# Kernel tuning notes

Hardware: AMD Instinct MI355X
Metric: run time of the kernel (lower is better)

Reference implementation:

```python
import jax, jax.numpy as jnp
import numpy as np

D = 1024
H = 16
HD = D // H
FF = 4 * D
LN_EPS = 1e-5


def _layernorm(x, w, b):
    mu = jnp.mean(x, axis=-1, keepdims=True)
    var = jnp.mean(jnp.square(x - mu), axis=-1, keepdims=True)
    return (x - mu) * jax.lax.rsqrt(var + LN_EPS) * w + b


def setup_inputs() -> dict:
    key = jax.random.key(0)
    ks = jax.random.split(key, 12)
    s = 0.02
    return {
        "x": jax.random.normal(ks[0], (8, 1024, D), jnp.float32),
        "c": jax.random.normal(ks[1], (8, D), jnp.float32),
        "ln1_w": jnp.ones((D,), jnp.float32),
        "ln1_b": jnp.zeros((D,), jnp.float32),
        "ln2_w": jnp.ones((D,), jnp.float32),
        "ln2_b": jnp.zeros((D,), jnp.float32),
        "ada_w": jax.random.normal(ks[2], (D, 6 * D), jnp.float32) * s,
        "ada_b": jnp.zeros((6 * D,), jnp.float32),
        "qkv_w": jax.random.normal(ks[3], (D, 3 * D), jnp.float32) * s,
        "qkv_b": jnp.zeros((3 * D,), jnp.float32),
        "proj_w": jax.random.normal(ks[4], (D, D), jnp.float32) * s,
        "proj_b": jnp.zeros((D,), jnp.float32),
        "fc1_w": jax.random.normal(ks[5], (D, FF), jnp.float32) * s,
        "fc1_b": jnp.zeros((FF,), jnp.float32),
        "fc2_w": jax.random.normal(ks[6], (FF, D), jnp.float32) * s,
        "fc2_b": jnp.zeros((D,), jnp.float32),
    }


def reference(x, c, ln1_w, ln1_b, ln2_w, ln2_b, ada_w, ada_b,
              qkv_w, qkv_b, proj_w, proj_b, fc1_w, fc1_b, fc2_w, fc2_b):
    B, L, _ = x.shape
    # adaLN modulation: SiLU(c) @ W -> 6 chunks of (B, D)
    ssg = jax.nn.silu(c) @ ada_w + ada_b
    msa_shift, msa_scale, msa_gate, mlp_shift, mlp_scale, mlp_gate = jnp.split(ssg, 6, axis=-1)

    def modulate(h, shift, scale):
        return h * (1.0 + scale[:, None, :]) + shift[:, None, :]

    # ---- attention branch ----
    h = modulate(_layernorm(x, ln1_w, ln1_b), msa_shift, msa_scale)
    qkv = h @ qkv_w + qkv_b                      # (B, L, 3D)
    q, k, v = jnp.split(qkv, 3, axis=-1)
    q = q.reshape(B, L, H, HD).transpose(0, 2, 1, 3)   # (B, H, L, HD)
    k = k.reshape(B, L, H, HD).transpose(0, 2, 1, 3)
    v = v.reshape(B, L, H, HD).transpose(0, 2, 1, 3)
    scores = jnp.einsum("bhqd,bhkd->bhqk", q, k) / jnp.sqrt(jnp.float32(HD))
    attn = jax.nn.softmax(scores, axis=-1)
    a = jnp.einsum("bhqk,bhkd->bhqd", attn, v)   # (B, H, L, HD)
    a = a.transpose(0, 2, 1, 3).reshape(B, L, D)
    a = a @ proj_w + proj_b
    x = x + msa_gate[:, None, :] * a

    # ---- MLP branch ----
    h = modulate(_layernorm(x, ln2_w, ln2_b), mlp_shift, mlp_scale)
    h = jax.nn.gelu(h @ fc1_w + fc1_b, approximate=True)
    h = h @ fc2_w + fc2_b
    x = x + mlp_gate[:, None, :] * h
    return x
```

## Files before the change

### kernel.cpp

```cpp
#include <hip/hip_runtime.h>
#include <math.h>

#define DMODEL 1024
#define SIXD   6144
#define NHEAD  16
#define HEADD  64
#define LSEQ   1024
#define NBATCH 8
#define MROWS  8192

typedef unsigned short ushort_t;
typedef __attribute__((ext_vector_type(8))) short bf16x8;
typedef __attribute__((ext_vector_type(4))) float f32x4;

__device__ __forceinline__ unsigned short f2bf(float f) {
  unsigned int u = __float_as_uint(f);
  u += 0x7fff + ((u >> 16) & 1);
  return (unsigned short)(u >> 16);
}

__device__ __forceinline__ void gload_lds16(const void* g, void* l) {
  __builtin_amdgcn_global_load_lds(
      (const __attribute__((address_space(1))) unsigned int*)g,
      (__attribute__((address_space(3))) unsigned int*)l, 16, 0, 0);
}

__global__ void tcast_kernel(const float* __restrict__ W, ushort_t* __restrict__ WT,
                             int K, int N) {
  __shared__ float tile[32][33];
  int tx = threadIdx.x & 31, ty = threadIdx.x >> 5;
  int n0 = blockIdx.x * 32, k0 = blockIdx.y * 32;
#pragma unroll
  for (int r = 0; r < 4; ++r)
    tile[ty + 8*r][tx] = W[(size_t)(k0 + ty + 8*r) * N + n0 + tx];
  __syncthreads();
#pragma unroll
  for (int r = 0; r < 4; ++r)
    WT[(size_t)(n0 + ty + 8*r) * K + k0 + tx] = f2bf(tile[tx][ty + 8*r]);
}

__global__ __launch_bounds__(256) void vtrans_kernel(
    const ushort_t* __restrict__ qkvb, ushort_t* __restrict__ vT) {
  __shared__ ushort_t tile[128][66];
  int bh = blockIdx.x;
  int kt = blockIdx.y;
  int b = bh >> 4, h = bh & 15;
  int tid = threadIdx.x;
#pragma unroll
  for (int i = 0; i < 4; ++i) {
    int flat = tid + 256 * i;
    int r = flat >> 3, c8 = flat & 7;
    bf16x8 v = *(const bf16x8*)((const short*)qkvb +
        (size_t)(b * LSEQ + kt * 128 + r) * 3072 + 2048 + h * 64 + c8 * 8);
#pragma unroll
    for (int j = 0; j < 8; ++j) tile[r][c8 * 8 + j] = (ushort_t)v[j];
  }
  __syncthreads();
#pragma unroll
  for (int i = 0; i < 4; ++i) {
    int d = i * 16 + (tid >> 4);
    int kc = tid & 15;
    bf16x8 ov;
#pragma unroll
    for (int j = 0; j < 8; ++j) ov[j] = (short)tile[kc * 8 + j][d];
    *(bf16x8*)((short*)vT + (size_t)(bh * 64 + d) * 1024 + kt * 128 + kc * 8) = ov;
  }
}

__global__ void ada_kernel(const float* __restrict__ c, const float* __restrict__ ada_w,
                           const float* __restrict__ ada_b, float* __restrict__ ssg) {
  __shared__ float s[DMODEL];
  int b = blockIdx.y;
  int j = blockIdx.x * 256 + threadIdx.x;
  for (int i = threadIdx.x; i < DMODEL; i += 256) {
    float v = c[b * DMODEL + i];
    s[i] = v / (1.0f + __expf(-v));
  }
  __syncthreads();
  float acc = ada_b[j];
#pragma unroll 8
  for (int k = 0; k < DMODEL; ++k)
    acc = fmaf(s[k], ada_w[(size_t)k * SIXD + j], acc);
  ssg[b * SIXD + j] = acc;
}

__global__ __launch_bounds__(256) void ln_mod_kernel(
    const float* __restrict__ xin, const float* __restrict__ lw,
    const float* __restrict__ lb, const float* __restrict__ ssg,
    int shift_off, int scale_off, ushort_t* __restrict__ outB) {
  int row = blockIdx.x;
  int b = row >> 10;
  int tid = threadIdx.x;
  float4 v = ((const float4*)xin)[(size_t)row * 256 + tid];
  float sum = v.x + v.y + v.z + v.w;
  float sq  = v.x*v.x + v.y*v.y + v.z*v.z + v.w*v.w;
#pragma unroll
  for (int m = 32; m; m >>= 1) { sum += __shfl_xor(sum, m); sq += __shfl_xor(sq, m); }
  __shared__ float rbuf[8];
  int w = tid >> 6, lane = tid & 63;
  if (lane == 0) { rbuf[w] = sum; rbuf[4 + w] = sq; }
  __syncthreads();
  sum = rbuf[0] + rbuf[1] + rbuf[2] + rbuf[3];
  sq  = rbuf[4] + rbuf[5] + rbuf[6] + rbuf[7];
  float mu  = sum * (1.0f / 1024.0f);
  float var = sq * (1.0f / 1024.0f) - mu * mu;
  float rs  = rsqrtf(var + 1e-5f);
  const float* sg = ssg + b * SIXD;
  float vv[4] = {v.x, v.y, v.z, v.w};
  ushort4 pk;
  unsigned short* pks = (unsigned short*)&pk;
#pragma unroll
  for (int j = 0; j < 4; ++j) {
    int d = tid * 4 + j;
    float h = (vv[j] - mu) * rs * lw[d] + lb[d];
    h = h * (1.0f + sg[scale_off + d]) + sg[shift_off + d];
    pks[j] = f2bf(h);
  }
  ((ushort4*)outB)[(size_t)row * 256 + tid] = pk;
}

template <int EPI>
__global__ __launch_bounds__(256, 2) void gemm_kernel(
    const ushort_t* __restrict__ A, const ushort_t* __restrict__ BT,
    const float* __restrict__ bias, const float* __restrict__ ssg,
    const float* resid, float* outF, ushort_t* __restrict__ outB,
    int N, int K, int gate_off, int gxs) {
  __shared__ __align__(16) char SM[65536];
  int tid = threadIdx.x, lane = tid & 63, w = tid >> 6;
  int l15 = lane & 15, g = lane >> 4;
  int orig = blockIdx.x;
  int xcd = orig & 7;
  int idx = orig >> 3;
  int bxi = idx & ((1 << gxs) - 1);
  int byl = (idx >> gxs) & 7;
  int bxg = idx >> (gxs + 3);
  int bx = (bxg << gxs) + bxi;
  int by = (xcd << 3) + byl;
  int m0 = by * 128, n0 = bx * 128;
  int wrow = (w >> 1) * 64, wcol = (w & 1) * 64;
  f32x4 zero = {0.f, 0.f, 0.f, 0.f};
  f32x4 acc[4][4];
#pragma unroll
  for (int i = 0; i < 4; ++i)
#pragma unroll
    for (int j = 0; j < 4; ++j) acc[i][j] = zero;

  const char* asrc[4];
  const char* bsrc[4];
#pragma unroll
  for (int ch = 0; ch < 4; ++ch) {
    int flat = ch * 4096 + tid * 16;
    int row = flat >> 7;
    int colb = (flat & 127) ^ ((row & 7) << 4);
    asrc[ch] = (const char*)A  + ((size_t)(m0 + row) * K) * 2 + colb;
    bsrc[ch] = (const char*)BT + ((size_t)(n0 + row) * K) * 2 + colb;
  }

  int T = K >> 6;
#pragma unroll
  for (int ch = 0; ch < 4; ++ch)
    gload_lds16(asrc[ch], SM + ch * 4096 + tid * 16);
#pragma unroll
  for (int ch = 0; ch < 4; ++ch)
    gload_lds16(bsrc[ch], SM + 16384 + ch * 4096 + tid * 16);

  for (int t = 0; t < T; ++t) {
    if (t + 1 < T) {
      char* base = SM + ((t + 1) & 1) * 32768;
      size_t ko = (size_t)(t + 1) * 128;
#pragma unroll
      for (int ch = 0; ch < 4; ++ch)
        gload_lds16(asrc[ch] + ko, base + ch * 4096 + tid * 16);
#pragma unroll
      for (int ch = 0; ch < 4; ++ch)
        gload_lds16(bsrc[ch] + ko, base + 16384 + ch * 4096 + tid * 16);
      asm volatile("s_waitcnt vmcnt(8)" ::: "memory");
    } else {
      asm volatile("s_waitcnt vmcnt(0)" ::: "memory");
    }
    asm volatile("s_barrier" ::: "memory");
    const char* ab = SM + (t & 1) * 32768;
    const char* bb = ab + 16384;
#pragma unroll
    for (int kk = 0; kk < 2; ++kk) {
      bf16x8 af[4], bfr[4];
#pragma unroll
      for (int i = 0; i < 4; ++i) {
        int ar = wrow + i * 16 + l15;
        af[i]  = *(const bf16x8*)(ab + ar * 128 + ((kk * 64 + g * 16) ^ ((ar & 7) << 4)));
        int br = wcol + i * 16 + l15;
        bfr[i] = *(const bf16x8*)(bb + br * 128 + ((kk * 64 + g * 16) ^ ((br & 7) << 4)));
      }
#pragma unroll
      for (int i = 0; i < 4; ++i)
#pragma unroll
        for (int j = 0; j < 4; ++j)
          acc[i][j] = __builtin_amdgcn_mfma_f32_16x16x32_bf16(af[i], bfr[j], acc[i][j], 0, 0, 0);
    }
    asm volatile("s_barrier" ::: "memory");
  }
#pragma unroll
  for (int i = 0; i < 4; ++i)
#pragma unroll
    for (int j = 0; j < 4; ++j)
#pragma unroll
      for (int r = 0; r < 4; ++r) {
        int grow = m0 + wrow + i * 16 + g * 4 + r;
        int gcol = n0 + wcol + j * 16 + l15;
        float v = acc[i][j][r] + bias[gcol];
        if (EPI == 0) {
          outB[(size_t)grow * N + gcol] = f2bf(v);
        } else if (EPI == 1 || EPI == 3) {
          int bb2 = grow >> 10;
          float gate = ssg[bb2 * SIXD + gate_off + gcol];
          size_t idx2 = (size_t)grow * N + gcol;
          outF[idx2] = resid[idx2] + gate * v;
        } else {
          float u = v;
          float t2 = 0.7978845608028654f * (u + 0.044715f * u * u * u);
          float e = __expf(2.0f * t2);
          float th = 1.0f - 2.0f / (e + 1.0f);
          outB[(size_t)grow * N + gcol] = f2bf(0.5f * u * (1.0f + th));
        }
      }
}

__global__ __launch_bounds__(256, 2) void attn_kernel(
    const ushort_t* __restrict__ qkv,
    const ushort_t* __restrict__ vT,
    ushort_t* __restrict__ aout) {
  __shared__ __align__(16) char SM[33024];
  float* lbuf = (float*)(SM + 32768);
  int tid = threadIdx.x, lane = tid & 63, w = tid >> 6;
  int l15 = lane & 15, g = lane >> 4;
  int qt = blockIdx.x, bh = blockIdx.y;
  int b = bh >> 4, h = bh & 15;
  const float sc = 0.18033688f;

  bf16x8 aq[2], aq2[2];
  {
    int qrow = qt * 128 + w * 16 + l15;
    const short* qp = (const short*)qkv + (size_t)(b * LSEQ + qrow) * 3072 + h * 64 + g * 8;
    aq[0] = *(const bf16x8*)qp;
    aq[1] = *(const bf16x8*)(qp + 32);
    const short* qp2 = qp + (size_t)64 * 3072;
    aq2[0] = *(const bf16x8*)qp2;
    aq2[1] = *(const bf16x8*)(qp2 + 32);
#pragma unroll
    for (int ks = 0; ks < 2; ++ks) {
#pragma unroll
      for (int s = 0; s < 2; ++s) {
        union { bf16x8 v; unsigned short u[8]; } qi, qo;
        qi.v = s ? aq2[ks] : aq[ks];
#pragma unroll
        for (int j = 0; j < 8; j += 2) {
          float lo = __uint_as_float((unsigned)qi.u[j] << 16) * sc;
          float hi = __uint_as_float((unsigned)qi.u[j + 1] << 16) * sc;
          unsigned pkd;
          asm("v_cvt_pk_bf16_f32 %0, %1, %2" : "=v"(pkd) : "v"(lo), "v"(hi));
          qo.u[j] = (unsigned short)(pkd & 0xffff);
          qo.u[j + 1] = (unsigned short)(pkd >> 16);
        }
        if (s) aq2[ks] = qo.v; else aq[ks] = qo.v;
      }
    }
  }

  const char* ksrc[2];
  const char* vsrc[2];
#pragma unroll
  for (int p = 0; p < 2; ++p) {
    int flat = p * 4096 + w * 1024 + lane * 16;
    int row = flat >> 7;
    int colb = (flat & 127) ^ ((row & 7) << 4);
    ksrc[p] = (const char*)qkv + ((size_t)(b * LSEQ + row) * 3072 + 1024 + h * 64) * 2 + colb;
    vsrc[p] = (const char*)vT + ((size_t)(bh * 64 + row) * 1024) * 2 + colb;
  }

  f32x4 zero = {0.f, 0.f, 0.f, 0.f};
  f32x4 o[4] = {zero, zero, zero, zero};
  f32x4 o2[4] = {zero, zero, zero, zero};
  float lrow = 0.f, lrow2 = 0.f;

#pragma unroll
  for (int p = 0; p < 2; ++p) {
    gload_lds16(ksrc[p], SM + p * 4096 + w * 1024);
    gload_lds16(vsrc[p], SM + 16384 + p * 4096 + w * 1024);
  }
  __syncthreads();

  for (int t = 0; t < 16; ++t) {
    int cur = t & 1;
    if (t < 15) {
      size_t koff = (size_t)(t + 1) * (64 * 3072 * 2);
      size_t voff = (size_t)(t + 1) * 128;
#pragma unroll
      for (int p = 0; p < 2; ++p) {
        gload_lds16(ksrc[p] + koff, SM + (cur ^ 1) * 8192 + p * 4096 + w * 1024);
        gload_lds16(vsrc[p] + voff, SM + 16384 + (cur ^ 1) * 8192 + p * 4096 + w * 1024);
      }
    }
    f32x4 s4[4] = {zero, zero, zero, zero};
    f32x4 s4b[4] = {zero, zero, zero, zero};
    __builtin_amdgcn_s_setprio(1);
#pragma unroll
    for (int c = 0; c < 4; ++c)
#pragma unroll
      for (int ks = 0; ks < 2; ++ks) {
        int key = c * 16 + l15;
        bf16x8 ak = *(const bf16x8*)(SM + cur * 8192 + key * 128 +
                                     ((ks * 64 + g * 16) ^ ((key & 7) << 4)));
        s4[c]  = __builtin_amdgcn_mfma_f32_16x16x32_bf16(ak, aq[ks],  s4[c],  0, 0, 0);
        s4b[c] = __builtin_amdgcn_mfma_f32_16x16x32_bf16(ak, aq2[ks], s4b[c], 0, 0, 0);
      }
    __builtin_amdgcn_s_setprio(0);
    unsigned pa[2][4], pa2[2][4];
    int gl = (g & 1) * 2;
#pragma unroll
    for (int s = 0; s < 2; ++s) {
      float p16[16], sump = 0.f;
#pragma unroll
      for (int c = 0; c < 4; ++c)
#pragma unroll
        for (int r = 0; r < 4; ++r) {
          float p = exp2f(s ? s4b[c][r] : s4[c][r]);
          p16[c * 4 + r] = p;
          sump += p;
        }
      sump += __shfl_xor(sump, 16);
      sump += __shfl_xor(sump, 32);
      if (s) lrow2 += sump; else lrow += sump;
      unsigned pk[8];
#pragma unroll
      for (int c = 0; c < 4; ++c)
#pragma unroll
        for (int m = 0; m < 2; ++m)
          asm("v_cvt_pk_bf16_f32 %0, %1, %2"
              : "=v"(pk[c * 2 + m]) : "v"(p16[c * 4 + 2 * m]), "v"(p16[c * 4 + 2 * m + 1]));
#pragma unroll
      for (int kb = 0; kb < 2; ++kb)
#pragma unroll
        for (int wv = 0; wv < 4; ++wv) {
          int srcl = l15 + (gl + (wv >> 1)) * 16;
          unsigned vA = (unsigned)__shfl((int)pk[kb * 4 + (wv & 1)], srcl);
          unsigned vB = (unsigned)__shfl((int)pk[kb * 4 + 2 + (wv & 1)], srcl);
          if (s) pa2[kb][wv] = (g >> 1) ? vB : vA;
          else   pa[kb][wv]  = (g >> 1) ? vB : vA;
        }
    }
    union PU { unsigned u[4]; bf16x8 v; };
    PU pu[2], pu2[2];
#pragma unroll
    for (int kb = 0; kb < 2; ++kb)
#pragma unroll
      for (int i = 0; i < 4; ++i) { pu[kb].u[i] = pa[kb][i]; pu2[kb].u[i] = pa2[kb][i]; }
    __builtin_amdgcn_s_setprio(1);
#pragma unroll
    for (int kb = 0; kb < 2; ++kb)
#pragma unroll
      for (int nb = 0; nb < 4; ++nb) {
        int d = nb * 16 + l15;
        bf16x8 bv = *(const bf16x8*)(SM + 16384 + cur * 8192 + d * 128 +
                                     ((kb * 64 + g * 16) ^ ((d & 7) << 4)));
        o[nb]  = __builtin_amdgcn_mfma_f32_16x16x32_bf16(pu[kb].v,  bv, o[nb],  0, 0, 0);
        o2[nb] = __builtin_amdgcn_mfma_f32_16x16x32_bf16(pu2[kb].v, bv, o2[nb], 0, 0, 0);
      }
    __builtin_amdgcn_s_setprio(0);
    __syncthreads();
  }
#pragma unroll
  for (int s = 0; s < 2; ++s) {
    float inv = 1.0f / (s ? lrow2 : lrow);
    if (lane < 16) lbuf[w * 16 + lane] = inv;
    f32x4 rl = *(const f32x4*)&lbuf[w * 16 + g * 4];
#pragma unroll
    for (int nb = 0; nb < 4; ++nb)
#pragma unroll
      for (int r = 0; r < 4; ++r) {
        int qrow = qt * 128 + s * 64 + w * 16 + g * 4 + r;
        const f32x4& oo = s ? o2[nb] : o[nb];
        aout[(size_t)(b * LSEQ + qrow) * 1024 + h * 64 + nb * 16 + l15] =
            f2bf(oo[r] * rl[r]);
      }
  }
}

extern "C" void kernel_launch(void* const* d_in, const int* in_sizes, int n_in,
                              void* d_out, int out_size, void* d_ws, size_t ws_size,
                              hipStream_t stream) {
  const float* x      = (const float*)d_in[0];
  const float* c      = (const float*)d_in[1];
  const float* ln1_w  = (const float*)d_in[2];
  const float* ln1_b  = (const float*)d_in[3];
  const float* ln2_w  = (const float*)d_in[4];
  const float* ln2_b  = (const float*)d_in[5];
  const float* ada_w  = (const float*)d_in[6];
  const float* ada_b  = (const float*)d_in[7];
  const float* qkv_w  = (const float*)d_in[8];
  const float* qkv_b  = (const float*)d_in[9];
  const float* proj_w = (const float*)d_in[10];
  const float* proj_b = (const float*)d_in[11];
  const float* fc1_w  = (const float*)d_in[12];
  const float* fc1_b  = (const float*)d_in[13];
  const float* fc2_w  = (const float*)d_in[14];
  const float* fc2_b  = (const float*)d_in[15];
  float* out = (float*)d_out;
  char* ws = (char*)d_ws;

  ushort_t* qkvT  = (ushort_t*)(ws + 0);
  ushort_t* projT = (ushort_t*)(ws + 6291456);
  ushort_t* fc1T  = (ushort_t*)(ws + 8388608);
  ushort_t* fc2T  = (ushort_t*)(ws + 16777216);
  float*    ssg   = (float*)(ws + 25165824);
  ushort_t* hbuf  = (ushort_t*)(ws + 25362432);
  ushort_t* abuf  = hbuf;
  ushort_t* qkvb  = (ushort_t*)(ws + 42139648);
  ushort_t* vTb   = (ushort_t*)(ws + 92471296);
  if (ws_size < (size_t)109248512) return;

  tcast_kernel<<<dim3(96, 32),  256, 0, stream>>>(qkv_w,  qkvT, 1024, 3072);
  tcast_kernel<<<dim3(32, 32),  256, 0, stream>>>(proj_w, projT, 1024, 1024);
  tcast_kernel<<<dim3(128, 32), 256, 0, stream>>>(fc1_w,  fc1T, 1024, 4096);
  tcast_kernel<<<dim3(32, 128), 256, 0, stream>>>(fc2_w,  fc2T, 4096, 1024);
  ada_kernel<<<dim3(24, 8), 256, 0, stream>>>(c, ada_w, ada_b, ssg);

  ln_mod_kernel<<<8192, 256, 0, stream>>>(x, ln1_w, ln1_b, ssg, 0, 1024, hbuf);
  gemm_kernel<0><<<1536, 256, 0, stream>>>(hbuf, qkvT, qkv_b, nullptr,
                                           nullptr, nullptr, qkvb, 3072, 1024, 0, 2);
  vtrans_kernel<<<dim3(128, 8), 256, 0, stream>>>(qkvb, vTb);
  attn_kernel<<<dim3(8, 128), 256, 0, stream>>>(qkvb, vTb, abuf);
  gemm_kernel<1><<<512, 256, 0, stream>>>(abuf, projT, proj_b, ssg,
                                          x, out, nullptr, 1024, 1024, 2048, 2);
  ln_mod_kernel<<<8192, 256, 0, stream>>>(out, ln2_w, ln2_b, ssg, 3072, 4096, hbuf);
  gemm_kernel<2><<<2048, 256, 0, stream>>>(hbuf, fc1T, fc1_b, nullptr,
                                           nullptr, nullptr, qkvb, 4096, 1024, 0, 2);
  gemm_kernel<3><<<512, 256, 0, stream>>>(qkvb, fc2T, fc2_b, ssg,
                                          out, out, nullptr, 1024, 4096, 5120, 1);
}
```

Baseline: 421.1 us.

## Triple-buffer K/V tiles in attention with explicit vmcnt waits and deferred row-sum reduce

Widens the attention kernel's K/V LDS staging from double to triple buffering. It prefetches two tiles ahead and replaces __syncthreads with explicit s_waitcnt vmcnt plus s_barrier, so the next loads stay in flight across the barrier. The cross-lane shuffle reduction of softmax row sums moves out of the inner loop to once at the end. LDS use rises to about 48KB per block, which could reduce occupancy, and the hand-written wait counts must match the number of outstanding loads.

```diff
diff --git a/kernel.cpp b/kernel.cpp
--- a/kernel.cpp
+++ b/kernel.cpp
@@ -229,8 +229,8 @@
     const ushort_t* __restrict__ qkv,
     const ushort_t* __restrict__ vT,
     ushort_t* __restrict__ aout) {
-  __shared__ __align__(16) char SM[33024];
-  float* lbuf = (float*)(SM + 32768);
+  __shared__ __align__(16) char SM[49408];
+  float* lbuf = (float*)(SM + 49152);
   int tid = threadIdx.x, lane = tid & 63, w = tid >> 6;
   int l15 = lane & 15, g = lane >> 4;
   int qt = blockIdx.x, bh = blockIdx.y;
@@ -277,29 +277,30 @@
     vsrc[p] = (const char*)vT + ((size_t)(bh * 64 + row) * 1024) * 2 + colb;
   }
 
+  auto STAGE = [&](int tt, int s) {
+    size_t koff = (size_t)tt * (64 * 3072 * 2);
+    size_t voff = (size_t)tt * 128;
+#pragma unroll
+    for (int p = 0; p < 2; ++p) {
+      gload_lds16(ksrc[p] + koff, SM + s * 8192 + p * 4096 + w * 1024);
+      gload_lds16(vsrc[p] + voff, SM + 24576 + s * 8192 + p * 4096 + w * 1024);
+    }
+  };
+
   f32x4 zero = {0.f, 0.f, 0.f, 0.f};
   f32x4 o[4] = {zero, zero, zero, zero};
   f32x4 o2[4] = {zero, zero, zero, zero};
   float lrow = 0.f, lrow2 = 0.f;
 
-#pragma unroll
-  for (int p = 0; p < 2; ++p) {
-    gload_lds16(ksrc[p], SM + p * 4096 + w * 1024);
-    gload_lds16(vsrc[p], SM + 16384 + p * 4096 + w * 1024);
-  }
-  __syncthreads();
-
+  STAGE(0, 0);
+  STAGE(1, 1);
+  asm volatile("s_waitcnt vmcnt(4)" ::: "memory");
+  asm volatile("s_barrier" ::: "memory");
+
+  int s0 = 0;
   for (int t = 0; t < 16; ++t) {
-    int cur = t & 1;
-    if (t < 15) {
-      size_t koff = (size_t)(t + 1) * (64 * 3072 * 2);
-      size_t voff = (size_t)(t + 1) * 128;
-#pragma unroll
-      for (int p = 0; p < 2; ++p) {
-        gload_lds16(ksrc[p] + koff, SM + (cur ^ 1) * 8192 + p * 4096 + w * 1024);
-        gload_lds16(vsrc[p] + voff, SM + 16384 + (cur ^ 1) * 8192 + p * 4096 + w * 1024);
-      }
-    }
+    int s2 = s0 + 2; if (s2 >= 3) s2 -= 3;
+    if (t + 2 < 16) STAGE(t + 2, s2);
     f32x4 s4[4] = {zero, zero, zero, zero};
     f32x4 s4b[4] = {zero, zero, zero, zero};
     __builtin_amdgcn_s_setprio(1);
@@ -308,7 +309,7 @@
 #pragma unroll
       for (int ks = 0; ks < 2; ++ks) {
         int key = c * 16 + l15;
-        bf16x8 ak = *(const bf16x8*)(SM + cur * 8192 + key * 128 +
+        bf16x8 ak = *(const bf16x8*)(SM + s0 * 8192 + key * 128 +
                                      ((ks * 64 + g * 16) ^ ((key & 7) << 4)));
         s4[c]  = __builtin_amdgcn_mfma_f32_16x16x32_bf16(ak, aq[ks],  s4[c],  0, 0, 0);
         s4b[c] = __builtin_amdgcn_mfma_f32_16x16x32_bf16(ak, aq2[ks], s4b[c], 0, 0, 0);
@@ -327,8 +328,6 @@
           p16[c * 4 + r] = p;
           sump += p;
         }
-      sump += __shfl_xor(sump, 16);
-      sump += __shfl_xor(sump, 32);
       if (s) lrow2 += sump; else lrow += sump;
       unsigned pk[8];
 #pragma unroll
@@ -360,14 +359,19 @@
 #pragma unroll
       for (int nb = 0; nb < 4; ++nb) {
         int d = nb * 16 + l15;
-        bf16x8 bv = *(const bf16x8*)(SM + 16384 + cur * 8192 + d * 128 +
+        bf16x8 bv = *(const bf16x8*)(SM + 24576 + s0 * 8192 + d * 128 +
                                      ((kb * 64 + g * 16) ^ ((d & 7) << 4)));
         o[nb]  = __builtin_amdgcn_mfma_f32_16x16x32_bf16(pu[kb].v,  bv, o[nb],  0, 0, 0);
         o2[nb] = __builtin_amdgcn_mfma_f32_16x16x32_bf16(pu2[kb].v, bv, o2[nb], 0, 0, 0);
       }
     __builtin_amdgcn_s_setprio(0);
-    __syncthreads();
-  }
+    if (t + 2 < 16)      asm volatile("s_waitcnt vmcnt(4)" ::: "memory");
+    else if (t + 1 < 16) asm volatile("s_waitcnt vmcnt(0)" ::: "memory");
+    if (t + 1 < 16)      asm volatile("s_barrier" ::: "memory");
+    s0 = s0 + 1; if (s0 >= 3) s0 -= 3;
+  }
+  lrow  += __shfl_xor(lrow, 16);  lrow  += __shfl_xor(lrow, 32);
+  lrow2 += __shfl_xor(lrow2, 16); lrow2 += __shfl_xor(lrow2, 32);
 #pragma unroll
   for (int s = 0; s < 2; ++s) {
     float inv = 1.0f / (s ? lrow2 : lrow);
```

Measured after the change: 415.7 us (median of 2 runs). No clear change (-1.3%).
